# Optimization experiments

Hardware: AMD Instinct MI355X
Metric: run time of the kernel (lower is better)

The kernel has to match this reference:

```python
import jax, jax.numpy as jnp
import numpy as np

# ---- config (matches init_kwargs: seek_thermal, K=1024 points, P=5 persons) ----
H, W = 150, 200
N = H * W
K = 1024          # max_num_points
P = 5             # max_num_persons
HFOV_DEG, VFOV_DEG = 81.0, 59.0
DEPTH_MIN = 3.0   # valid depth threshold
BIG = 1e9         # sentinel for invalid depths when sorting


def _camera_rays():
    fx = W / (2.0 * np.tan(np.deg2rad(HFOV_DEG) / 2.0))
    fy = H / (2.0 * np.tan(np.deg2rad(VFOV_DEG) / 2.0))
    x, y = np.meshgrid(np.arange(W, dtype=np.float32), np.arange(H, dtype=np.float32), indexing='xy')
    x_cam = (x - W / 2.0) / fx   # (H, W)
    y_cam = (y - H / 2.0) / fy   # (H, W)
    return jnp.asarray(x_cam), jnp.asarray(y_cam)


def _masked_quantile(d_sorted, n, q):
    # linear-interpolation quantile over the first n sorted entries (torch.quantile default)
    pos = q * jnp.maximum(n.astype(d_sorted.dtype) - 1.0, 0.0)          # (B, P)
    lo = jnp.floor(pos).astype(jnp.int32)
    hi = jnp.ceil(pos).astype(jnp.int32)
    frac = pos - lo.astype(d_sorted.dtype)
    vlo = jnp.take_along_axis(d_sorted, lo[..., None], axis=-1)[..., 0]
    vhi = jnp.take_along_axis(d_sorted, hi[..., None], axis=-1)[..., 0]
    return vlo + (vhi - vlo) * frac


def setup_inputs() -> dict:
    key = jax.random.key(0)
    k1, k2, k3 = jax.random.split(key, 3)
    B = 128
    depth = jax.random.uniform(k1, (B, H, W), dtype=jnp.float32) * 8.0            # depths 0..8m
    indicator = jax.random.randint(k2, (B, H, W), 0, P + 1).astype(jnp.float32)   # person ids 0..P
    extra = jax.random.normal(k3, (B, H, W), dtype=jnp.float32)                   # unused channel
    depth_mask_3C = jnp.stack([depth, indicator, extra], axis=1)                  # (B, 3, H, W)
    return {"depth_mask_3C": depth_mask_3C}


def reference(depth_mask_3C) -> jnp.ndarray:
    B = depth_mask_3C.shape[0]
    dtype = depth_mask_3C.dtype
    x_cam, y_cam = _camera_rays()

    depth = depth_mask_3C[:, 0].reshape(B, N)                         # (B, N)
    indicator = jnp.round(depth_mask_3C[:, 1]).reshape(B, N)          # (B, N)

    # per-person membership masks, persons 1..P
    pids = jnp.arange(1, P + 1, dtype=dtype)
    mask = indicator[:, None, :] == pids[None, :, None]               # (B, P, N)
    valid = mask & (depth[:, None, :] > DEPTH_MIN)                    # (B, P, N)

    # grouped IQR outlier bounds via masked sort + interpolated quantile
    d = jnp.where(valid, depth[:, None, :], BIG)
    d_sorted = jnp.sort(d, axis=-1)                                   # (B, P, N)
    n_valid = valid.sum(axis=-1)                                      # (B, P)
    q1 = _masked_quantile(d_sorted, n_valid, 0.25)
    q3 = _masked_quantile(d_sorted, n_valid, 0.75)
    iqr = q3 - q1
    lb = (q1 - 1.5 * iqr)[..., None]
    ub = (q3 + 1.5 * iqr)[..., None]
    keep = valid & (depth[:, None, :] >= lb) & (depth[:, None, :] <= ub)   # (B, P, N)

    # 3D points: (x_cam*z, y_cam*z, z) per pixel
    rays = jnp.stack([x_cam.reshape(N), y_cam.reshape(N), jnp.ones((N,), dtype)], axis=-1)  # (N, 3)
    pts = depth[..., None] * rays[None]                               # (B, N, 3)

    # deterministic variant of sampling: take the first K kept points in raster order
    rank = jnp.cumsum(keep.astype(jnp.int32), axis=-1) - 1            # (B, P, N)
    idx = jnp.where(keep & (rank < K), rank, K)                       # overflow/invalid -> slot K (discarded)

    def fill(idx_p, pts_b):                                           # idx_p (N,), pts_b (N, 3)
        return jnp.zeros((K + 1, 3), dtype).at[idx_p].set(pts_b)[:K]

    buf = jax.vmap(lambda i_b, p_b: jax.vmap(fill, in_axes=(0, None))(i_b, p_b))(idx, pts)  # (B, P, K, 3)

    # presence flag goes into slot K, channel 0
    flag = (keep.sum(axis=-1) > 0).astype(dtype)                      # (B, P)
    extra = flag[..., None, None] * jnp.array([1.0, 0.0, 0.0], dtype) # (B, P, 1, 3)
    seg = jnp.concatenate([buf, extra], axis=2)                       # (B, P, K+1, 3)
    return jnp.transpose(seg, (0, 3, 1, 2)).reshape(B, 3, P * (K + 1))
```

## Files before the change

### kernel.cpp

```cpp
#include <hip/hip_runtime.h>
#include <math.h>

#define HGT 150
#define WID 200
#define NPIX 30000
#define NF4  7500
#define KMAX 1024
#define PMAX 5
#define CAP  4096
#define NW   938
#define NBIN 1024
#define GCAP 128
#define STRIDE_C (PMAX*(KMAX+1))

__device__ __forceinline__ uint32_t wave_incl_scan(uint32_t x, int lane) {
#pragma unroll
    for (int off = 1; off < 64; off <<= 1) {
        uint32_t y = __shfl_up(x, (unsigned)off, 64);
        if (lane >= off) x += y;
    }
    return x;
}
__device__ __forceinline__ uint32_t wave_red_add(uint32_t x) {
#pragma unroll
    for (int off = 32; off >= 1; off >>= 1) x += __shfl_xor(x, off, 64);
    return x;
}
__device__ __forceinline__ uint32_t wave_red_min(uint32_t x) {
#pragma unroll
    for (int off = 32; off >= 1; off >>= 1) { uint32_t y = __shfl_xor(x, off, 64); x = y < x ? y : x; }
    return x;
}
__device__ __forceinline__ uint32_t wave_red_max(uint32_t x) {
#pragma unroll
    for (int off = 32; off >= 1; off >>= 1) { uint32_t y = __shfl_xor(x, off, 64); x = y > x ? y : x; }
    return x;
}

__device__ void locate_ranks(const uint32_t* hh, int seg,
                             const uint32_t* s_rank, const uint32_t* s_base,
                             uint32_t* s_tbin, uint32_t* s_tbel, uint32_t* s_ws) {
    const int tid = threadIdx.x, lane = tid & 63, wv = tid >> 6;
    const uint32_t* mine = hh + tid * seg;
    uint32_t segsum = 0;
    for (int j = 0; j < seg; ++j) segsum += mine[j];
    uint32_t inc = wave_incl_scan(segsum, lane);
    if (lane == 63) s_ws[wv] = inc;
    __syncthreads();
    uint32_t tbase = inc - segsum;
    for (int w = 0; w < wv; ++w) tbase += s_ws[w];
#pragma unroll
    for (int k = 0; k < 4; ++k) {
        uint32_t r = s_rank[k] - s_base[k];
        if (r >= tbase && r < tbase + segsum) {
            uint32_t c = tbase;
            for (int j = 0; j < seg; ++j) {
                uint32_t h = mine[j];
                if (r < c + h) { s_tbin[k] = (uint32_t)(tid * seg + j); s_tbel[k] = c; break; }
                c += h;
            }
        }
    }
    __syncthreads();
}

__global__ __launch_bounds__(256, 4) void fused(const float* __restrict__ in,
                                                float* __restrict__ out, int B) {
    const int nbp = B * PMAX;
    int x = blockIdx.x, b, p;
    if ((nbp & 7) == 0) {
        int per = nbp >> 3;
        int slot = (x & 7) * per + (x >> 3);
        b = slot / PMAX; p = slot - b * PMAX;
    } else { b = x / PMAX; p = x - b * PMAX; }

    const float pid = (float)(p + 1);
    const float4* __restrict__ depth4 = (const float4*)(in + (size_t)b * 3 * NPIX);
    const float4* __restrict__ ind4   = depth4 + NF4;
    const int tid = threadIdx.x, lane = tid & 63, wv = tid >> 6;

    __shared__ uint32_t keys[CAP];
    __shared__ unsigned short sidx[CAP];
    __shared__ uint32_t hist[NBIN];
    __shared__ uint32_t vb2[NW];
    __shared__ unsigned short wpfx[NW];
    __shared__ float xc_tab[WID];
    __shared__ float yc_tab[HGT];
    __shared__ uint32_t gbuf[4 * GCAP];
    __shared__ uint32_t gcnt[4];
    __shared__ uint32_t s_ws[4];
    __shared__ uint32_t s_mm[8];
    __shared__ uint32_t s_rank[4], s_base[4], s_tbin[4], s_tbel[4], s_u[4], s_val[4];
    __shared__ int s_slot[4], s_desc[4];
    __shared__ uint32_t s_dprefix, s_dr;
    __shared__ float s_lbub[2];

    for (int i = tid; i < NBIN; i += 256) hist[i] = 0;
    for (int i = tid; i < NW; i += 256) vb2[i] = 0;
    {
        const double fxd = (double)WID / (2.0 * tan((81.0 * M_PI / 180.0) * 0.5));
        const double fyd = (double)HGT / (2.0 * tan((59.0 * M_PI / 180.0) * 0.5));
        for (int i = tid; i < WID; i += 256) xc_tab[i] = (float)(((double)i - (double)WID / 2.0) / fxd);
        for (int i = tid; i < HGT; i += 256) yc_tab[i] = (float)(((double)i - (double)HGT / 2.0) / fyd);
    }

    uint32_t m[4] = {0u, 0u, 0u, 0u};
    uint32_t cnt = 0, kmn = 0xFFFFFFFFu, kmx = 0u;
#pragma unroll 6
    for (int k = 0; k < 30; ++k) {
        int f = k * 256 + tid;
        if (f < NF4) {
            float4 d4 = depth4[f];
            float4 i4 = ind4[f];
            const float* dd = (const float*)&d4;
            const float* ii = (const float*)&i4;
            uint32_t nib = 0;
#pragma unroll
            for (int j = 0; j < 4; ++j)
                if (rintf(ii[j]) == pid && dd[j] > 3.0f) {
                    nib |= 1u << j;
                    uint32_t key = __float_as_uint(dd[j]);
                    kmn = key < kmn ? key : kmn;
                    kmx = key > kmx ? key : kmx;
                }
            cnt += (uint32_t)__popc(nib);
            m[k >> 3] |= nib << (4 * (k & 7));
        }
    }
    {
        uint32_t inc = wave_incl_scan(cnt, lane);
        uint32_t wmn = wave_red_min(kmn), wmx = wave_red_max(kmx);
        if (lane == 63) s_ws[wv] = inc;
        if (lane == 0) { s_mm[wv] = wmn; s_mm[4 + wv] = wmx; }
        __syncthreads();
        uint32_t bacc = inc - cnt;
        for (int w = 0; w < wv; ++w) bacc += s_ws[w];
        cnt = bacc;
        kmn = s_mm[0]; kmx = s_mm[4];
#pragma unroll
        for (int w = 1; w < 4; ++w) {
            kmn = s_mm[w] < kmn ? s_mm[w] : kmn;
            kmx = s_mm[4 + w] > kmx ? s_mm[4 + w] : kmx;
        }
    }
    const uint32_t n = s_ws[0] + s_ws[1] + s_ws[2] + s_ws[3];
    const uint32_t mybase = cnt;

    float* outB = out + (size_t)b * 3 * STRIDE_C + p * (KMAX + 1);

    if (n == 0) {
        for (int r = tid; r <= KMAX; r += 256) {
            outB[r] = 0.f; outB[STRIDE_C + r] = 0.f; outB[2 * STRIDE_C + r] = 0.f;
        }
        return;
    }

    uint32_t rank[4]; float posf[2];
    {
        float nf = (float)n;
        posf[0] = 0.25f * fmaxf(nf - 1.0f, 0.0f);
        posf[1] = 0.75f * fmaxf(nf - 1.0f, 0.0f);
        rank[0] = (uint32_t)floorf(posf[0]); rank[1] = (uint32_t)ceilf(posf[0]);
        rank[2] = (uint32_t)floorf(posf[1]); rank[3] = (uint32_t)ceilf(posf[1]);
    }

    if (n > CAP) {
        uint32_t v[4];
        for (int k = 0; k < 4; ++k) {
            if (tid == 0) { s_dprefix = 0; s_dr = rank[k]; }
            __syncthreads();
            for (int bit = 30; bit >= 0; --bit) {
                uint32_t pfx = s_dprefix;
                uint32_t c = 0;
                for (int kk = 0; kk < 30; ++kk) {
                    int f = kk * 256 + tid;
                    if (f < NF4) {
                        float4 d4 = depth4[f]; float4 i4 = ind4[f];
                        const float* dd = (const float*)&d4;
                        const float* ii = (const float*)&i4;
#pragma unroll
                        for (int j = 0; j < 4; ++j)
                            if (rintf(ii[j]) == pid && dd[j] > 3.0f) {
                                uint32_t key = __float_as_uint(dd[j]);
                                if ((key >> (bit + 1)) == pfx && !((key >> bit) & 1u)) ++c;
                            }
                    }
                }
                c = wave_red_add(c);
                if (lane == 0) s_ws[wv] = c;
                __syncthreads();
                uint32_t c0 = s_ws[0] + s_ws[1] + s_ws[2] + s_ws[3];
                if (tid == 0) {
                    if (s_dr < c0) s_dprefix = pfx << 1;
                    else { s_dprefix = (pfx << 1) | 1u; s_dr -= c0; }
                }
                __syncthreads();
            }
            v[k] = s_dprefix;
            __syncthreads();
        }
        float f1 = posf[0] - floorf(posf[0]);
        float f3 = posf[1] - floorf(posf[1]);
        float q1 = __uint_as_float(v[0]) + (__uint_as_float(v[1]) - __uint_as_float(v[0])) * f1;
        float q3 = __uint_as_float(v[2]) + (__uint_as_float(v[3]) - __uint_as_float(v[2])) * f3;
        float iqr = q3 - q1;
        float lb = q1 - 1.5f * iqr, ub = q3 + 1.5f * iqr;
        if (tid == 0) {
            const float* depth = (const float*)depth4;
            const float* ind = (const float*)ind4;
            uint32_t r = 0;
            for (int i = 0; i < NPIX; ++i) {
                float d = depth[i];
                if (rintf(ind[i]) == pid && d > 3.0f && d >= lb && d <= ub) {
                    if (r < KMAX) {
                        int row = i / WID, col = i - row * WID;
                        outB[r] = xc_tab[col] * d;
                        outB[STRIDE_C + r] = yc_tab[row] * d;
                        outB[2 * STRIDE_C + r] = d;
                    }
                    ++r;
                }
            }
            s_dr = r;
        }
        __syncthreads();
        uint32_t count = s_dr;
        uint32_t start = count < KMAX ? count : KMAX;
        for (uint32_t r = start + tid; r < KMAX; r += 256) {
            outB[r] = 0.f; outB[STRIDE_C + r] = 0.f; outB[2 * STRIDE_C + r] = 0.f;
        }
        if (tid == 0) {
            outB[KMAX] = (count > 0) ? 1.0f : 0.0f;
            outB[STRIDE_C + KMAX] = 0.f; outB[2 * STRIDE_C + KMAX] = 0.f;
        }
        return;
    }

    {
        uint32_t pos = mybase;
#pragma unroll 6
        for (int k = 0; k < 30; ++k) {
            uint32_t nib = (m[k >> 3] >> (4 * (k & 7))) & 0xFu;
            if (nib) {
                int f = k * 256 + tid;
                float4 d4 = depth4[f];
                const float* dd = (const float*)&d4;
#pragma unroll
                for (int j = 0; j < 4; ++j)
                    if ((nib >> j) & 1u) {
                        keys[pos] = __float_as_uint(dd[j]);
                        sidx[pos] = (unsigned short)(f * 4 + j);
                        ++pos;
                    }
            }
        }
        if (tid == 0) {
#pragma unroll
            for (int k = 0; k < 4; ++k) { s_rank[k] = rank[k]; s_base[k] = 0; }
        }
        __syncthreads();
    }

    const uint32_t span = kmx - kmn;
    const bool exact = (span < NBIN);
    uint32_t scale = 0;
    if (!exact) scale = (uint32_t)(((uint64_t)NBIN << 32) / ((uint64_t)span + 1));

    for (uint32_t i = tid; i < n; i += 256) {
        uint32_t key = keys[i];
        uint32_t bin = exact ? (key - kmn)
                             : (uint32_t)(((uint64_t)(key - kmn) * scale) >> 32);
        atomicAdd(&hist[bin], 1u);
    }
    __syncthreads();
    locate_ranks(hist, NBIN / 256, s_rank, s_base, s_tbin, s_tbel, s_ws);

    if (tid == 0) {
        if (exact) {
#pragma unroll
            for (int k = 0; k < 4; ++k) s_val[k] = kmn + s_tbin[k];
        } else {
            uint32_t uq[4]; int nu = 0;
#pragma unroll
            for (int k = 0; k < 4; ++k) {
                s_base[k] = s_tbel[k];
                int fnd = -1;
                for (int u = 0; u < nu; ++u) if (uq[u] == s_tbin[k]) fnd = u;
                if (fnd < 0) { uq[nu] = s_tbin[k]; fnd = nu; ++nu; }
                s_slot[k] = fnd;
            }
#pragma unroll
            for (int u = 0; u < 4; ++u) { s_u[u] = 0xFFFFFFFFu; gcnt[u] = 0; }
            for (int u = 0; u < nu; ++u) if (hist[uq[u]] <= GCAP) s_u[u] = uq[u];
#pragma unroll
            for (int k = 0; k < 4; ++k) s_desc[k] = (hist[uq[s_slot[k]]] > GCAP) ? 1 : 0;
        }
    }
    __syncthreads();

    if (!exact) {
        for (uint32_t i = tid; i < n; i += 256) {
            uint32_t key = keys[i];
            uint32_t bin = (uint32_t)(((uint64_t)(key - kmn) * scale) >> 32);
#pragma unroll
            for (int u = 0; u < 4; ++u)
                if (bin == s_u[u]) {
                    uint32_t slot = atomicAdd(&gcnt[u], 1u);
                    if (slot < GCAP) gbuf[u * GCAP + slot] = key;
                }
        }
        __syncthreads();
        if (wv < 4 && !s_desc[wv]) {
            int u = s_slot[wv];
            uint32_t c = gcnt[u];
            uint32_t res = s_rank[wv] - s_base[wv];
            for (uint32_t i = lane; i < c; i += 64) {
                uint32_t xk = gbuf[u * GCAP + i];
                uint32_t less = 0, eq = 0;
                for (uint32_t j = 0; j < c; ++j) {
                    uint32_t y = gbuf[u * GCAP + j];
                    less += (y < xk); eq += (y == xk);
                }
                if (res >= less && res < less + eq) s_val[wv] = xk;
            }
        }
        __syncthreads();
        for (int k = 0; k < 4; ++k) if (s_desc[k]) {
            if (tid == 0) { s_dprefix = 0; s_dr = s_rank[k]; }
            __syncthreads();
            for (int bit = 30; bit >= 0; --bit) {
                uint32_t pfx = s_dprefix;
                uint32_t c = 0;
                for (uint32_t i = tid; i < n; i += 256) {
                    uint32_t key = keys[i];
                    if ((key >> (bit + 1)) == pfx && !((key >> bit) & 1u)) ++c;
                }
                c = wave_red_add(c);
                if (lane == 0) s_ws[wv] = c;
                __syncthreads();
                uint32_t c0 = s_ws[0] + s_ws[1] + s_ws[2] + s_ws[3];
                if (tid == 0) {
                    if (s_dr < c0) s_dprefix = pfx << 1;
                    else { s_dprefix = (pfx << 1) | 1u; s_dr -= c0; }
                }
                __syncthreads();
            }
            if (tid == 0) s_val[k] = s_dprefix;
            __syncthreads();
        }
    }

    if (tid == 0) {
        float f1 = posf[0] - floorf(posf[0]);
        float f3 = posf[1] - floorf(posf[1]);
        float v0 = __uint_as_float(s_val[0]), v1 = __uint_as_float(s_val[1]);
        float v2 = __uint_as_float(s_val[2]), v3 = __uint_as_float(s_val[3]);
        float q1 = v0 + (v1 - v0) * f1;
        float q3 = v2 + (v3 - v2) * f3;
        float iqr = q3 - q1;
        s_lbub[0] = q1 - 1.5f * iqr;
        s_lbub[1] = q3 + 1.5f * iqr;
    }
    __syncthreads();

    const float lb = s_lbub[0], ub = s_lbub[1];
    for (uint32_t i = tid; i < n; i += 256) {
        float d = __uint_as_float(keys[i]);
        if (d >= lb && d <= ub) {
            int s = sidx[i];
            atomicOr(&vb2[s >> 5], 1u << (s & 31));
        }
    }
    __syncthreads();
    uint32_t pc[4] = {0, 0, 0, 0};
    uint32_t lsum = 0;
    const int w0 = tid * 4;
#pragma unroll
    for (int j = 0; j < 4; ++j)
        if (w0 + j < NW) { pc[j] = (uint32_t)__popc(vb2[w0 + j]); lsum += pc[j]; }
    {
        uint32_t inc = wave_incl_scan(lsum, lane);
        if (lane == 63) s_ws[wv] = inc;
        __syncthreads();
        uint32_t tb = inc - lsum;
        for (int w = 0; w < wv; ++w) tb += s_ws[w];
        uint32_t run = tb;
#pragma unroll
        for (int j = 0; j < 4; ++j)
            if (w0 + j < NW) { wpfx[w0 + j] = (unsigned short)run; run += pc[j]; }
    }
    __syncthreads();
    const uint32_t total = s_ws[0] + s_ws[1] + s_ws[2] + s_ws[3];

    for (uint32_t i = tid; i < n; i += 256) {
        uint32_t key = keys[i];
        float d = __uint_as_float(key);
        if (d >= lb && d <= ub) {
            int s = sidx[i];
            int w = s >> 5;
            uint32_t r = (uint32_t)wpfx[w] + (uint32_t)__popc(vb2[w] & ((1u << (s & 31)) - 1u));
            if (r < KMAX) {
                int row = s / WID;
                int col = s - row * WID;
                outB[r] = xc_tab[col] * d;
                outB[STRIDE_C + r] = yc_tab[row] * d;
                outB[2 * STRIDE_C + r] = d;
            }
        }
    }
    uint32_t start = total < KMAX ? total : KMAX;
    for (uint32_t r = start + tid; r < KMAX; r += 256) {
        outB[r] = 0.f; outB[STRIDE_C + r] = 0.f; outB[2 * STRIDE_C + r] = 0.f;
    }
    if (tid == 0) {
        outB[KMAX] = (total > 0) ? 1.0f : 0.0f;
        outB[STRIDE_C + KMAX] = 0.f;
        outB[2 * STRIDE_C + KMAX] = 0.f;
    }
}

extern "C" void kernel_launch(void* const* d_in, const int* in_sizes, int n_in,
                              void* d_out, int out_size, void* d_ws, size_t ws_size,
                              hipStream_t stream) {
    (void)n_in; (void)out_size; (void)d_ws; (void)ws_size;
    const float* in = (const float*)d_in[0];
    float* out = (float*)d_out;
    const int B = in_sizes[0] / (3 * NPIX);
    fused<<<B * PMAX, 256, 0, stream>>>(in, out, B);
}
```

Before: 116.4 us.

## Build point list and fixed-range histogram in one pass with 512 threads

```diff
diff --git a/kernel.cpp b/kernel.cpp
--- a/kernel.cpp
+++ b/kernel.cpp
@@ -7,9 +7,14 @@
 #define NF4  7500
 #define KMAX 1024
 #define PMAX 5
+#define THREADS 512
+#define NWAVES 8
 #define CAP  4096
-#define NW   938
-#define NBIN 1024
+#define NWORDS 938
+#define NWPAD 940
+#define NBIN 2048
+#define SHIFT 13
+#define KBASE 0x40400000u
 #define GCAP 128
 #define STRIDE_C (PMAX*(KMAX+1))
 
@@ -26,19 +31,12 @@
     for (int off = 32; off >= 1; off >>= 1) x += __shfl_xor(x, off, 64);
     return x;
 }
-__device__ __forceinline__ uint32_t wave_red_min(uint32_t x) {
-#pragma unroll
-    for (int off = 32; off >= 1; off >>= 1) { uint32_t y = __shfl_xor(x, off, 64); x = y < x ? y : x; }
-    return x;
-}
-__device__ __forceinline__ uint32_t wave_red_max(uint32_t x) {
-#pragma unroll
-    for (int off = 32; off >= 1; off >>= 1) { uint32_t y = __shfl_xor(x, off, 64); x = y > x ? y : x; }
-    return x;
-}
-
-__device__ void locate_ranks(const uint32_t* hh, int seg,
-                             const uint32_t* s_rank, const uint32_t* s_base,
+__device__ __forceinline__ uint32_t key_bin(uint32_t key) {
+    uint32_t d = (key - KBASE) >> SHIFT;
+    return d < NBIN ? d : (NBIN - 1);
+}
+
+__device__ void locate_ranks(const uint32_t* hh, int seg, const uint32_t* s_rank,
                              uint32_t* s_tbin, uint32_t* s_tbel, uint32_t* s_ws) {
     const int tid = threadIdx.x, lane = tid & 63, wv = tid >> 6;
     const uint32_t* mine = hh + tid * seg;
@@ -51,7 +49,7 @@
     for (int w = 0; w < wv; ++w) tbase += s_ws[w];
 #pragma unroll
     for (int k = 0; k < 4; ++k) {
-        uint32_t r = s_rank[k] - s_base[k];
+        uint32_t r = s_rank[k];
         if (r >= tbase && r < tbase + segsum) {
             uint32_t c = tbase;
             for (int j = 0; j < seg; ++j) {
@@ -64,8 +62,8 @@
     __syncthreads();
 }
 
-__global__ __launch_bounds__(256, 4) void fused(const float* __restrict__ in,
-                                                float* __restrict__ out, int B) {
+__global__ __launch_bounds__(THREADS, 4) void fused(const float* __restrict__ in,
+                                                    float* __restrict__ out, int B) {
     const int nbp = B * PMAX;
     int x = blockIdx.x, b, p;
     if ((nbp & 7) == 0) {
@@ -79,77 +77,71 @@
     const float4* __restrict__ ind4   = depth4 + NF4;
     const int tid = threadIdx.x, lane = tid & 63, wv = tid >> 6;
 
-    __shared__ uint32_t keys[CAP];
-    __shared__ unsigned short sidx[CAP];
+    __shared__ uint2 list[CAP];
     __shared__ uint32_t hist[NBIN];
-    __shared__ uint32_t vb2[NW];
-    __shared__ unsigned short wpfx[NW];
+    __shared__ uint32_t vb2[NWPAD];
+    __shared__ unsigned short wpfx[NWPAD];
     __shared__ float xc_tab[WID];
     __shared__ float yc_tab[HGT];
     __shared__ uint32_t gbuf[4 * GCAP];
     __shared__ uint32_t gcnt[4];
-    __shared__ uint32_t s_ws[4];
-    __shared__ uint32_t s_mm[8];
-    __shared__ uint32_t s_rank[4], s_base[4], s_tbin[4], s_tbel[4], s_u[4], s_val[4];
+    __shared__ uint32_t s_ws[NWAVES];
+    __shared__ uint32_t s_rank[4], s_res[4], s_tbin[4], s_tbel[4], s_u[4], s_val[4];
     __shared__ int s_slot[4], s_desc[4];
-    __shared__ uint32_t s_dprefix, s_dr;
+    __shared__ uint32_t s_cnt, s_dprefix, s_dr;
     __shared__ float s_lbub[2];
 
-    for (int i = tid; i < NBIN; i += 256) hist[i] = 0;
-    for (int i = tid; i < NW; i += 256) vb2[i] = 0;
+    for (int i = tid; i < NBIN; i += THREADS) hist[i] = 0;
+    for (int i = tid; i < NWPAD; i += THREADS) vb2[i] = 0;
+    if (tid == 0) s_cnt = 0;
     {
         const double fxd = (double)WID / (2.0 * tan((81.0 * M_PI / 180.0) * 0.5));
         const double fyd = (double)HGT / (2.0 * tan((59.0 * M_PI / 180.0) * 0.5));
-        for (int i = tid; i < WID; i += 256) xc_tab[i] = (float)(((double)i - (double)WID / 2.0) / fxd);
-        for (int i = tid; i < HGT; i += 256) yc_tab[i] = (float)(((double)i - (double)HGT / 2.0) / fyd);
-    }
-
-    uint32_t m[4] = {0u, 0u, 0u, 0u};
-    uint32_t cnt = 0, kmn = 0xFFFFFFFFu, kmx = 0u;
-#pragma unroll 6
-    for (int k = 0; k < 30; ++k) {
-        int f = k * 256 + tid;
+        for (int i = tid; i < WID; i += THREADS) xc_tab[i] = (float)(((double)i - (double)WID / 2.0) / fxd);
+        for (int i = tid; i < HGT; i += THREADS) yc_tab[i] = (float)(((double)i - (double)HGT / 2.0) / fyd);
+    }
+    __syncthreads();
+
+#pragma unroll 5
+    for (int k = 0; k < 15; ++k) {
+        int f = k * THREADS + tid;
+        uint32_t nib = 0;
+        float4 d4;
         if (f < NF4) {
-            float4 d4 = depth4[f];
+            d4 = depth4[f];
             float4 i4 = ind4[f];
             const float* dd = (const float*)&d4;
             const float* ii = (const float*)&i4;
-            uint32_t nib = 0;
 #pragma unroll
             for (int j = 0; j < 4; ++j)
-                if (rintf(ii[j]) == pid && dd[j] > 3.0f) {
-                    nib |= 1u << j;
+                if (rintf(ii[j]) == pid && dd[j] > 3.0f) nib |= 1u << j;
+        }
+        uint32_t cnt_t = (uint32_t)__popc(nib);
+        uint32_t incl = wave_incl_scan(cnt_t, lane);
+        uint32_t wtot = __shfl(incl, 63, 64);
+        uint32_t base = 0;
+        if (lane == 63 && wtot) base = atomicAdd(&s_cnt, wtot);
+        base = __shfl(base, 63, 64);
+        uint32_t pos = base + incl - cnt_t;
+        if (nib) {
+            const float* dd = (const float*)&d4;
+#pragma unroll
+            for (int j = 0; j < 4; ++j)
+                if ((nib >> j) & 1u) {
                     uint32_t key = __float_as_uint(dd[j]);
-                    kmn = key < kmn ? key : kmn;
-                    kmx = key > kmx ? key : kmx;
+                    atomicAdd(&hist[key_bin(key)], 1u);
+                    if (pos < CAP) list[pos] = make_uint2(key, (uint32_t)(f * 4 + j));
+                    ++pos;
                 }
-            cnt += (uint32_t)__popc(nib);
-            m[k >> 3] |= nib << (4 * (k & 7));
-        }
-    }
-    {
-        uint32_t inc = wave_incl_scan(cnt, lane);
-        uint32_t wmn = wave_red_min(kmn), wmx = wave_red_max(kmx);
-        if (lane == 63) s_ws[wv] = inc;
-        if (lane == 0) { s_mm[wv] = wmn; s_mm[4 + wv] = wmx; }
-        __syncthreads();
-        uint32_t bacc = inc - cnt;
-        for (int w = 0; w < wv; ++w) bacc += s_ws[w];
-        cnt = bacc;
-        kmn = s_mm[0]; kmx = s_mm[4];
-#pragma unroll
-        for (int w = 1; w < 4; ++w) {
-            kmn = s_mm[w] < kmn ? s_mm[w] : kmn;
-            kmx = s_mm[4 + w] > kmx ? s_mm[4 + w] : kmx;
-        }
-    }
-    const uint32_t n = s_ws[0] + s_ws[1] + s_ws[2] + s_ws[3];
-    const uint32_t mybase = cnt;
+        }
+    }
+    __syncthreads();
+    const uint32_t n = s_cnt;
 
     float* outB = out + (size_t)b * 3 * STRIDE_C + p * (KMAX + 1);
 
     if (n == 0) {
-        for (int r = tid; r <= KMAX; r += 256) {
+        for (int r = tid; r <= KMAX; r += THREADS) {
             outB[r] = 0.f; outB[STRIDE_C + r] = 0.f; outB[2 * STRIDE_C + r] = 0.f;
         }
         return;
@@ -172,8 +164,8 @@
             for (int bit = 30; bit >= 0; --bit) {
                 uint32_t pfx = s_dprefix;
                 uint32_t c = 0;
-                for (int kk = 0; kk < 30; ++kk) {
-                    int f = kk * 256 + tid;
+                for (int kk = 0; kk < 15; ++kk) {
+                    int f = kk * THREADS + tid;
                     if (f < NF4) {
                         float4 d4 = depth4[f]; float4 i4 = ind4[f];
                         const float* dd = (const float*)&d4;
@@ -189,7 +181,8 @@
                 c = wave_red_add(c);
                 if (lane == 0) s_ws[wv] = c;
                 __syncthreads();
-                uint32_t c0 = s_ws[0] + s_ws[1] + s_ws[2] + s_ws[3];
+                uint32_t c0 = 0;
+                for (int w = 0; w < NWAVES; ++w) c0 += s_ws[w];
                 if (tid == 0) {
                     if (s_dr < c0) s_dprefix = pfx << 1;
                     else { s_dprefix = (pfx << 1) | 1u; s_dr -= c0; }
@@ -226,7 +219,7 @@
         __syncthreads();
         uint32_t count = s_dr;
         uint32_t start = count < KMAX ? count : KMAX;
-        for (uint32_t r = start + tid; r < KMAX; r += 256) {
+        for (uint32_t r = start + tid; r < KMAX; r += THREADS) {
             outB[r] = 0.f; outB[STRIDE_C + r] = 0.f; outB[2 * STRIDE_C + r] = 0.f;
         }
         if (tid == 0) {
@@ -236,118 +229,80 @@
         return;
     }
 
-    {
-        uint32_t pos = mybase;
-#pragma unroll 6
-        for (int k = 0; k < 30; ++k) {
-            uint32_t nib = (m[k >> 3] >> (4 * (k & 7))) & 0xFu;
-            if (nib) {
-                int f = k * 256 + tid;
-                float4 d4 = depth4[f];
-                const float* dd = (const float*)&d4;
-#pragma unroll
-                for (int j = 0; j < 4; ++j)
-                    if ((nib >> j) & 1u) {
-                        keys[pos] = __float_as_uint(dd[j]);
-                        sidx[pos] = (unsigned short)(f * 4 + j);
-                        ++pos;
-                    }
-            }
-        }
-        if (tid == 0) {
-#pragma unroll
-            for (int k = 0; k < 4; ++k) { s_rank[k] = rank[k]; s_base[k] = 0; }
-        }
+    if (tid == 0) {
+#pragma unroll
+        for (int k = 0; k < 4; ++k) s_rank[k] = rank[k];
+    }
+    __syncthreads();
+    locate_ranks(hist, NBIN / THREADS, s_rank, s_tbin, s_tbel, s_ws);
+
+    if (tid == 0) {
+        uint32_t uq[4]; int nu = 0;
+#pragma unroll
+        for (int k = 0; k < 4; ++k) {
+            s_res[k] = rank[k] - s_tbel[k];
+            int fnd = -1;
+            for (int u = 0; u < nu; ++u) if (uq[u] == s_tbin[k]) fnd = u;
+            if (fnd < 0) { uq[nu] = s_tbin[k]; fnd = nu; ++nu; }
+            s_slot[k] = fnd;
+        }
+#pragma unroll
+        for (int u = 0; u < 4; ++u) { s_u[u] = 0xFFFFFFFFu; gcnt[u] = 0; }
+        for (int u = 0; u < nu; ++u) if (hist[uq[u]] <= GCAP) s_u[u] = uq[u];
+#pragma unroll
+        for (int k = 0; k < 4; ++k) s_desc[k] = (hist[uq[s_slot[k]]] > GCAP) ? 1 : 0;
+    }
+    __syncthreads();
+
+    for (uint32_t i = tid; i < n; i += THREADS) {
+        uint32_t key = list[i].x;
+        uint32_t bin = key_bin(key);
+#pragma unroll
+        for (int u = 0; u < 4; ++u)
+            if (bin == s_u[u]) {
+                uint32_t slot = atomicAdd(&gcnt[u], 1u);
+                if (slot < GCAP) gbuf[u * GCAP + slot] = key;
+            }
+    }
+    __syncthreads();
+    if (wv < 4 && !s_desc[wv]) {
+        int u = s_slot[wv];
+        uint32_t c = gcnt[u];
+        uint32_t res = s_res[wv];
+        for (uint32_t i = lane; i < c; i += 64) {
+            uint32_t xk = gbuf[u * GCAP + i];
+            uint32_t less = 0, eq = 0;
+            for (uint32_t j = 0; j < c; ++j) {
+                uint32_t y = gbuf[u * GCAP + j];
+                less += (y < xk); eq += (y == xk);
+            }
+            if (res >= less && res < less + eq) s_val[wv] = xk;
+        }
+    }
+    __syncthreads();
+    for (int k = 0; k < 4; ++k) if (s_desc[k]) {
+        if (tid == 0) { s_dprefix = 0; s_dr = rank[k]; }
         __syncthreads();
-    }
-
-    const uint32_t span = kmx - kmn;
-    const bool exact = (span < NBIN);
-    uint32_t scale = 0;
-    if (!exact) scale = (uint32_t)(((uint64_t)NBIN << 32) / ((uint64_t)span + 1));
-
-    for (uint32_t i = tid; i < n; i += 256) {
-        uint32_t key = keys[i];
-        uint32_t bin = exact ? (key - kmn)
-                             : (uint32_t)(((uint64_t)(key - kmn) * scale) >> 32);
-        atomicAdd(&hist[bin], 1u);
-    }
-    __syncthreads();
-    locate_ranks(hist, NBIN / 256, s_rank, s_base, s_tbin, s_tbel, s_ws);
-
-    if (tid == 0) {
-        if (exact) {
-#pragma unroll
-            for (int k = 0; k < 4; ++k) s_val[k] = kmn + s_tbin[k];
-        } else {
-            uint32_t uq[4]; int nu = 0;
-#pragma unroll
-            for (int k = 0; k < 4; ++k) {
-                s_base[k] = s_tbel[k];
-                int fnd = -1;
-                for (int u = 0; u < nu; ++u) if (uq[u] == s_tbin[k]) fnd = u;
-                if (fnd < 0) { uq[nu] = s_tbin[k]; fnd = nu; ++nu; }
-                s_slot[k] = fnd;
-            }
-#pragma unroll
-            for (int u = 0; u < 4; ++u) { s_u[u] = 0xFFFFFFFFu; gcnt[u] = 0; }
-            for (int u = 0; u < nu; ++u) if (hist[uq[u]] <= GCAP) s_u[u] = uq[u];
-#pragma unroll
-            for (int k = 0; k < 4; ++k) s_desc[k] = (hist[uq[s_slot[k]]] > GCAP) ? 1 : 0;
-        }
-    }
-    __syncthreads();
-
-    if (!exact) {
-        for (uint32_t i = tid; i < n; i += 256) {
-            uint32_t key = keys[i];
-            uint32_t bin = (uint32_t)(((uint64_t)(key - kmn) * scale) >> 32);
-#pragma unroll
-            for (int u = 0; u < 4; ++u)
-                if (bin == s_u[u]) {
-                    uint32_t slot = atomicAdd(&gcnt[u], 1u);
-                    if (slot < GCAP) gbuf[u * GCAP + slot] = key;
-                }
-        }
+        for (int bit = 30; bit >= 0; --bit) {
+            uint32_t pfx = s_dprefix;
+            uint32_t c = 0;
+            for (uint32_t i = tid; i < n; i += THREADS) {
+                uint32_t key = list[i].x;
+                if ((key >> (bit + 1)) == pfx && !((key >> bit) & 1u)) ++c;
+            }
+            c = wave_red_add(c);
+            if (lane == 0) s_ws[wv] = c;
+            __syncthreads();
+            uint32_t c0 = 0;
+            for (int w = 0; w < NWAVES; ++w) c0 += s_ws[w];
+            if (tid == 0) {
+                if (s_dr < c0) s_dprefix = pfx << 1;
+                else { s_dprefix = (pfx << 1) | 1u; s_dr -= c0; }
+            }
+            __syncthreads();
+        }
+        if (tid == 0) s_val[k] = s_dprefix;
         __syncthreads();
-        if (wv < 4 && !s_desc[wv]) {
-            int u = s_slot[wv];
-            uint32_t c = gcnt[u];
-            uint32_t res = s_rank[wv] - s_base[wv];
-            for (uint32_t i = lane; i < c; i += 64) {
-                uint32_t xk = gbuf[u * GCAP + i];
-                uint32_t less = 0, eq = 0;
-                for (uint32_t j = 0; j < c; ++j) {
-                    uint32_t y = gbuf[u * GCAP + j];
-                    less += (y < xk); eq += (y == xk);
-                }
-                if (res >= less && res < less + eq) s_val[wv] = xk;
-            }
-        }
-        __syncthreads();
-        for (int k = 0; k < 4; ++k) if (s_desc[k]) {
-            if (tid == 0) { s_dprefix = 0; s_dr = s_rank[k]; }
-            __syncthreads();
-            for (int bit = 30; bit >= 0; --bit) {
-                uint32_t pfx = s_dprefix;
-                uint32_t c = 0;
-                for (uint32_t i = tid; i < n; i += 256) {
-                    uint32_t key = keys[i];
-                    if ((key >> (bit + 1)) == pfx && !((key >> bit) & 1u)) ++c;
-                }
-                c = wave_red_add(c);
-                if (lane == 0) s_ws[wv] = c;
-                __syncthreads();
-                uint32_t c0 = s_ws[0] + s_ws[1] + s_ws[2] + s_ws[3];
-                if (tid == 0) {
-                    if (s_dr < c0) s_dprefix = pfx << 1;
-                    else { s_dprefix = (pfx << 1) | 1u; s_dr -= c0; }
-                }
-                __syncthreads();
-            }
-            if (tid == 0) s_val[k] = s_dprefix;
-            __syncthreads();
-        }
     }
 
     if (tid == 0) {
@@ -364,44 +319,46 @@
     __syncthreads();
 
     const float lb = s_lbub[0], ub = s_lbub[1];
-    for (uint32_t i = tid; i < n; i += 256) {
-        float d = __uint_as_float(keys[i]);
-        if (d >= lb && d <= ub) {
-            int s = sidx[i];
-            atomicOr(&vb2[s >> 5], 1u << (s & 31));
-        }
-    }
-    __syncthreads();
-    uint32_t pc[4] = {0, 0, 0, 0};
-    uint32_t lsum = 0;
-    const int w0 = tid * 4;
-#pragma unroll
-    for (int j = 0; j < 4; ++j)
-        if (w0 + j < NW) { pc[j] = (uint32_t)__popc(vb2[w0 + j]); lsum += pc[j]; }
+    for (uint32_t i = tid; i < n; i += THREADS) {
+        uint2 e = list[i];
+        float d = __uint_as_float(e.x);
+        if (d >= lb && d <= ub) atomicOr(&vb2[e.y >> 5], 1u << (e.y & 31));
+    }
+    __syncthreads();
     {
+        uint4 v4 = make_uint4(0, 0, 0, 0);
+        if (tid < NWPAD / 4) v4 = ((const uint4*)vb2)[tid];
+        uint32_t pc0 = (uint32_t)__popc(v4.x), pc1 = (uint32_t)__popc(v4.y);
+        uint32_t pc2 = (uint32_t)__popc(v4.z), pc3 = (uint32_t)__popc(v4.w);
+        uint32_t lsum = pc0 + pc1 + pc2 + pc3;
         uint32_t inc = wave_incl_scan(lsum, lane);
         if (lane == 63) s_ws[wv] = inc;
         __syncthreads();
-        uint32_t tb = inc - lsum;
-        for (int w = 0; w < wv; ++w) tb += s_ws[w];
-        uint32_t run = tb;
-#pragma unroll
-        for (int j = 0; j < 4; ++j)
-            if (w0 + j < NW) { wpfx[w0 + j] = (unsigned short)run; run += pc[j]; }
-    }
-    __syncthreads();
-    const uint32_t total = s_ws[0] + s_ws[1] + s_ws[2] + s_ws[3];
-
-    for (uint32_t i = tid; i < n; i += 256) {
-        uint32_t key = keys[i];
-        float d = __uint_as_float(key);
+        uint32_t run = inc - lsum;
+        for (int w = 0; w < wv; ++w) run += s_ws[w];
+        if (tid < NWPAD / 4) {
+            ushort4 w4;
+            w4.x = (unsigned short)run;            run += pc0;
+            w4.y = (unsigned short)run;            run += pc1;
+            w4.z = (unsigned short)run;            run += pc2;
+            w4.w = (unsigned short)run;
+            ((ushort4*)wpfx)[tid] = w4;
+        }
+    }
+    __syncthreads();
+    uint32_t total = 0;
+    for (int w = 0; w < NWAVES; ++w) total += s_ws[w];
+
+    for (uint32_t i = tid; i < n; i += THREADS) {
+        uint2 e = list[i];
+        float d = __uint_as_float(e.x);
         if (d >= lb && d <= ub) {
-            int s = sidx[i];
-            int w = s >> 5;
+            uint32_t s = e.y;
+            uint32_t w = s >> 5;
             uint32_t r = (uint32_t)wpfx[w] + (uint32_t)__popc(vb2[w] & ((1u << (s & 31)) - 1u));
             if (r < KMAX) {
-                int row = s / WID;
-                int col = s - row * WID;
+                uint32_t row = s / WID;
+                uint32_t col = s - row * WID;
                 outB[r] = xc_tab[col] * d;
                 outB[STRIDE_C + r] = yc_tab[row] * d;
                 outB[2 * STRIDE_C + r] = d;
@@ -409,7 +366,7 @@
         }
     }
     uint32_t start = total < KMAX ? total : KMAX;
-    for (uint32_t r = start + tid; r < KMAX; r += 256) {
+    for (uint32_t r = start + tid; r < KMAX; r += THREADS) {
         outB[r] = 0.f; outB[STRIDE_C + r] = 0.f; outB[2 * STRIDE_C + r] = 0.f;
     }
     if (tid == 0) {
@@ -426,5 +383,5 @@
     const float* in = (const float*)d_in[0];
     float* out = (float*)d_out;
     const int B = in_sizes[0] / (3 * NPIX);
-    fused<<<B * PMAX, 256, 0, stream>>>(in, out, B);
-}
+    fused<<<B * PMAX, THREADS, 0, stream>>>(in, out, B);
+}
```

Result: faster. 101.5 us (-12.8%).
